# Performance work log

Hardware: AMD Instinct MI355X
Metric: run time of the kernel (lower is better)

Reference implementation:

```python
import jax, jax.numpy as jnp
import numpy as np

B, N, D = 8, 1024, 768
H, Y, M = 12, 64, 3072  # heads, head_dim, hopfield memories (4*D)
STEPS = 12
ALPHA = 0.1
EPS = 1e-5


def setup_inputs() -> dict:
    key = jax.random.key(0)
    k0, k1, k2, k3 = jax.random.split(key, 4)
    return {
        "x": jax.random.normal(k0, (B, N, D), dtype=jnp.float32),
        "gamma": jnp.ones((D,), dtype=jnp.float32),
        "beta_ln": jnp.zeros((D,), dtype=jnp.float32),
        "Wq": jax.random.normal(k1, (H, Y, D), dtype=jnp.float32) / np.float32(np.sqrt(D)),
        "Wk": jax.random.normal(k2, (H, Y, D), dtype=jnp.float32) / np.float32(np.sqrt(D)),
        "xi": jax.random.normal(k3, (M, D), dtype=jnp.float32) / np.float32(np.sqrt(D)),
    }


def _layernorm(x, gamma, beta_ln):
    mu = jnp.mean(x, axis=-1, keepdims=True)
    var = jnp.var(x, axis=-1, keepdims=True)
    return gamma * (x - mu) * jax.lax.rsqrt(var + EPS) + beta_ln


def _energy(g, Wq, Wk, xi):
    # Energy attention: E^ATT = -(1/beta) * sum_{h,q} logsumexp_k(beta * <K_hk, Q_hq>)
    q = jnp.einsum('hyd,bnd->bhny', Wq, g)
    k = jnp.einsum('hyd,bnd->bhny', Wk, g)
    beta = jnp.asarray(1.0 / np.sqrt(Y), g.dtype)
    scores = beta * jnp.einsum('bhky,bhqy->bhkq', k, q)  # [B,H,N_k,N_q]
    e_att = -(1.0 / beta) * jnp.sum(jax.nn.logsumexp(scores, axis=2))
    # Hopfield energy: E^HN = -0.5 * sum relu(g @ xi^T)^2
    h = jnp.einsum('bnd,md->bnm', g, xi)
    e_hn = -0.5 * jnp.sum(jnp.square(jax.nn.relu(h)))
    return e_att + e_hn


def reference(x, gamma, beta_ln, Wq, Wk, xi):
    grad_e = jax.grad(_energy)
    def step(xc, _):
        g = _layernorm(xc, gamma, beta_ln)
        # gradient taken at g (not chained through LayerNorm), then SGD update
        xc = xc - ALPHA * grad_e(g, Wq, Wk, xi)
        return xc, None
    out, _ = jax.lax.scan(step, x, None, length=STEPS)
    return out
```

## Files before the change

### kernel.cpp

```cpp
#include <hip/hip_runtime.h>
#include <math.h>

#define H_ 12
#define STEPS_ 12
#define ALPHA_ 0.1f
#define EPS_ 1e-5f
#define BETA_ 0.125f
#define NTOK 8192

typedef unsigned short u16;
typedef __attribute__((ext_vector_type(8))) u16 u16x8;
typedef __attribute__((ext_vector_type(4))) u16 u16x4;
typedef __attribute__((ext_vector_type(4))) float f32x4;
typedef __attribute__((ext_vector_type(8))) __bf16 bf16x8;

#define MFMA __builtin_amdgcn_mfma_f32_16x16x32_bf16

__device__ __forceinline__ u16 f2bf(float x) {
    unsigned u = __float_as_uint(x);
    u += 0x7FFFu + ((u >> 16) & 1u);
    return (u16)(u >> 16);
}
__device__ __forceinline__ float bf2f(u16 u) {
    return __uint_as_float(((unsigned)u) << 16);
}

__device__ __forceinline__ void gl2lds16(const u16* gsrc, u16* ldst) {
    __builtin_amdgcn_global_load_lds(
        (const __attribute__((address_space(1))) void*)gsrc,
        (__attribute__((address_space(3))) void*)ldst, 16, 0, 0);
}

#define RAW_BARRIER()   asm volatile("s_barrier" ::: "memory")
#define WAIT_VM(n)      asm volatile("s_waitcnt vmcnt(" #n ")" ::: "memory")

__global__ __launch_bounds__(256) void ln_kernel(const float* __restrict__ x,
    const float* __restrict__ gamma, const float* __restrict__ beta,
    u16* __restrict__ g)
{
    int row = blockIdx.x;
    const float* xr = x + (size_t)row * 768;
    u16* gr = g + (size_t)row * 768;
    int t = threadIdx.x;
    float v0 = xr[t], v1 = xr[t + 256], v2 = xr[t + 512];
    float s = v0 + v1 + v2;
    #pragma unroll
    for (int off = 32; off > 0; off >>= 1) s += __shfl_down(s, off);
    __shared__ float red[8];
    int wid = t >> 6, lane = t & 63;
    if (lane == 0) red[wid] = s;
    __syncthreads();
    if (t == 0) red[0] = (red[0] + red[1] + red[2] + red[3]) * (1.0f / 768.0f);
    __syncthreads();
    float mu = red[0];
    float d0 = v0 - mu, d1 = v1 - mu, d2 = v2 - mu;
    float ss = d0*d0 + d1*d1 + d2*d2;
    #pragma unroll
    for (int off = 32; off > 0; off >>= 1) ss += __shfl_down(ss, off);
    if (lane == 0) red[4 + wid] = ss;
    __syncthreads();
    if (t == 0) red[4] = rsqrtf((red[4] + red[5] + red[6] + red[7]) * (1.0f / 768.0f) + EPS_);
    __syncthreads();
    float rs = red[4];
    gr[t]       = f2bf(gamma[t]       * d0 * rs + beta[t]);
    gr[t + 256] = f2bf(gamma[t + 256] * d1 * rs + beta[t + 256]);
    gr[t + 512] = f2bf(gamma[t + 512] * d2 * rs + beta[t + 512]);
}

__global__ __launch_bounds__(192) void reduce_ln(const u16* __restrict__ part,
    float* __restrict__ xc, const float* __restrict__ gamma,
    const float* __restrict__ beta, u16* __restrict__ g)
{
    int row = blockIdx.x, t = threadIdx.x;
    const u16x4* p0 = (const u16x4*)(part + (size_t)row * 768);
    const u16x4* p1 = (const u16x4*)(part + (size_t)(8192 + row) * 768);
    f32x4* xr = (f32x4*)(xc + (size_t)row * 768);
    f32x4 v = xr[t];
    u16x4 a = p0[t], b = p1[t];
    #pragma unroll
    for (int e = 0; e < 4; ++e) v[e] = fmaf(ALPHA_, bf2f(a[e]) + bf2f(b[e]), v[e]);
    xr[t] = v;
    float s = (v[0] + v[1]) + (v[2] + v[3]);
    #pragma unroll
    for (int off = 32; off > 0; off >>= 1) s += __shfl_down(s, off);
    __shared__ float red[8];
    int wid = t >> 6, lane = t & 63;
    if (lane == 0) red[wid] = s;
    __syncthreads();
    if (t == 0) red[0] = (red[0] + red[1] + red[2]) * (1.0f / 768.0f);
    __syncthreads();
    float mu = red[0];
    f32x4 d;
    #pragma unroll
    for (int e = 0; e < 4; ++e) d[e] = v[e] - mu;
    float ss = (d[0]*d[0] + d[1]*d[1]) + (d[2]*d[2] + d[3]*d[3]);
    #pragma unroll
    for (int off = 32; off > 0; off >>= 1) ss += __shfl_down(ss, off);
    if (lane == 0) red[4 + wid] = ss;
    __syncthreads();
    if (t == 0) red[4] = rsqrtf((red[4] + red[5] + red[6]) * (1.0f / 768.0f) + EPS_);
    __syncthreads();
    float rs = red[4];
    const f32x4 gm = *(const f32x4*)&gamma[t * 4];
    const f32x4 bt = *(const f32x4*)&beta[t * 4];
    u16x4 o;
    #pragma unroll
    for (int e = 0; e < 4; ++e) o[e] = f2bf(fmaf(gm[e], d[e] * rs, bt[e]));
    *(u16x4*)&g[(size_t)row * 768 + t * 4] = o;
}

__global__ __launch_bounds__(256) void convert_bf(const float* __restrict__ src,
                                                  u16* __restrict__ dst, int n4)
{
    int i = blockIdx.x * 256 + threadIdx.x;
    if (i < n4) {
        f32x4 v = *(const f32x4*)&src[i * 4];
        u16x4 o;
        #pragma unroll
        for (int e = 0; e < 4; ++e) o[e] = f2bf(v[e]);
        *(u16x4*)&dst[i * 4] = o;
    }
}

__global__ __launch_bounds__(256) void transpose_bf(const float* __restrict__ Wq,
    const float* __restrict__ Wk, const float* __restrict__ xi, u16* __restrict__ out)
{
    __shared__ float tile[64][65];
    int rb = blockIdx.x * 64, cb = blockIdx.y * 64;
    const float* src;
    if (rb < 768) src = Wq + (size_t)rb * 768;
    else if (rb < 1536) src = Wk + (size_t)(rb - 768) * 768;
    else src = xi + (size_t)(rb - 1536) * 768;
    int t = threadIdx.x;
    #pragma unroll
    for (int it = 0; it < 4; ++it) {
        int r = (t >> 4) + 16 * it;
        f32x4 v = *(const f32x4*)&src[(size_t)r * 768 + cb + (t & 15) * 4];
        #pragma unroll
        for (int e = 0; e < 4; ++e) tile[r][(t & 15) * 4 + e] = v[e];
    }
    __syncthreads();
    #pragma unroll
    for (int it = 0; it < 4; ++it) {
        int cl = (t >> 4) + 16 * it;
        u16x4 o;
        #pragma unroll
        for (int e = 0; e < 4; ++e) o[e] = f2bf(tile[(t & 15) * 4 + e][cl]);
        *(u16x4*)&out[(size_t)(cb + cl) * 4608 + rb + (t & 15) * 4] = o;
    }
}

__global__ __launch_bounds__(512) void gemm_fwd(
    const u16* __restrict__ A,
    const u16* __restrict__ Bt,
    u16* __restrict__ qkb, u16* __restrict__ qkT, u16* __restrict__ midb)
{
    __shared__ __align__(16) u16 S[2][12288];
    const int t = threadIdx.x, w = t >> 6, l = t & 63, g = l >> 4, cid = l & 15;
    const int lr = l & 15, lc = l >> 4;
    const int flat = blockIdx.x;
    const int xcd = flat & 7, slot = flat >> 3;
    const int nid = slot / 4, mloc = slot % 4;
    const int bm = (xcd * 4 + mloc) * 256;
    const int bn = nid * 128;
    const int RO = (w >> 1) * 64, CO = (w & 1) * 64;
    f32x4 acc[4][4] = {};

    const u16* gp[3];
    int ld[3];
    #pragma unroll
    for (int j = 0; j < 3; ++j) {
        int c = 3 * w + j;
        if (c < 16) {
            gp[j] = A + (size_t)(bm + 16 * c + lr) * 768 + 8 * lc;
            ld[j] = (64 * c + l) * 8;
        } else {
            gp[j] = Bt + (size_t)(bn + 16 * (c - 16) + lr) * 768 + 8 * lc;
            ld[j] = 8192 + (64 * (c - 16) + l) * 8;
        }
    }

    auto stage = [&](int buf, int off) {
        #pragma unroll
        for (int j = 0; j < 3; ++j)
            gl2lds16(gp[j] + off, &S[buf][ld[j]]);
    };
    auto compute = [&](int buf) {
        bf16x8 af[4], bfr[4];
        #pragma unroll
        for (int i = 0; i < 4; ++i) af[i]  = *(const bf16x8*)&S[buf][(64 * ((RO >> 4) + i) + l) * 8];
        #pragma unroll
        for (int j = 0; j < 4; ++j) bfr[j] = *(const bf16x8*)&S[buf][8192 + (64 * ((CO >> 4) + j) + l) * 8];
        #pragma unroll
        for (int i = 0; i < 4; ++i)
            #pragma unroll
            for (int j = 0; j < 4; ++j)
                acc[i][j] = MFMA(af[i], bfr[j], acc[i][j], 0, 0, 0);
    };
    auto adv = [&]() { gp[0] += 64; gp[1] += 64; gp[2] += 64; };

    stage(0, 0); stage(1, 32);
    #pragma unroll 1
    for (int ii = 0; ii < 11; ++ii) {
        WAIT_VM(3); RAW_BARRIER(); compute(0); RAW_BARRIER(); stage(0, 64);
        WAIT_VM(3); RAW_BARRIER(); compute(1); RAW_BARRIER(); stage(1, 96);
        adv();
    }
    WAIT_VM(3); RAW_BARRIER(); compute(0);
    WAIT_VM(0); RAW_BARRIER(); compute(1);

    if (bn < 1536) {
        int bidx = bm >> 10;
        #pragma unroll
        for (int i = 0; i < 4; ++i) {
            int tok = bm + RO + 16 * i + 4 * g;
            #pragma unroll
            for (int j = 0; j < 4; ++j) {
                int col = bn + CO + 16 * j + cid;
                int sel = col >= 768 ? 1 : 0;
                int cc = col - 768 * sel;
                int hh = cc >> 6, yy = cc & 63;
                u16x4 tv;
                #pragma unroll
                for (int r = 0; r < 4; ++r) {
                    u16 bv = f2bf(acc[i][j][r]);
                    tv[r] = bv;
                    qkb[(size_t)(tok + r) * 1536 + col] = bv;
                }
                *(u16x4*)&qkT[((((size_t)bidx * 12 + hh) * 2 + sel) * 64 + yy) * 1024 + (tok & 1023)] = tv;
            }
        }
    } else {
        #pragma unroll
        for (int i = 0; i < 4; ++i)
            #pragma unroll
            for (int r = 0; r < 4; ++r) {
                size_t row = bm + RO + 16 * i + 4 * g + r;
                #pragma unroll
                for (int j = 0; j < 4; ++j) {
                    int col = bn + CO + 16 * j + cid;
                    midb[row * 4608 + col] = f2bf(fmaxf(acc[i][j][r], 0.0f));
                }
            }
    }
}

__global__ __launch_bounds__(256, 4) void gemm_upd(
    const u16* __restrict__ A,
    const u16* __restrict__ Bt,
    u16* __restrict__ part)
{
    __shared__ __align__(16) u16 As[2][4096];
    __shared__ __align__(16) u16 Bs[2][4096];
    const int t = threadIdx.x, w = t >> 6, l = t & 63, g = l >> 4, cid = l & 15;
    const int lr = l & 15, lc = l >> 4;
    const int flat = blockIdx.x;
    const int xcd = flat & 7, slot = flat >> 3;
    const int z = slot / 48, rem = slot % 48;
    const int mloc = rem / 6, n = rem % 6;
    const int bm = ((xcd << 3) + mloc) * 128, bn = n * 128;
    const int kbeg = z * 2304;
    const int RO = (w >> 1) * 64, CO = (w & 1) * 64;
    u16* out = part + (size_t)z * 8192 * 768;
    f32x4 acc[4][4] = {};

    const u16* ga0 = A  + (size_t)(bm + 32 * w + lr) * 4608 + kbeg + 8 * lc;
    const u16* ga1 = A  + (size_t)(bm + 32 * w + 16 + lr) * 4608 + kbeg + 8 * lc;
    const u16* gb0 = Bt + (size_t)(bn + 32 * w + lr) * 4608 + kbeg + 8 * lc;
    const u16* gb1 = Bt + (size_t)(bn + 32 * w + 16 + lr) * 4608 + kbeg + 8 * lc;

    auto stage = [&](int buf, int off) {
        gl2lds16(ga0 + off, &As[buf][(64 * (2 * w + 0) + l) * 8]);
        gl2lds16(ga1 + off, &As[buf][(64 * (2 * w + 1) + l) * 8]);
        gl2lds16(gb0 + off, &Bs[buf][(64 * (2 * w + 0) + l) * 8]);
        gl2lds16(gb1 + off, &Bs[buf][(64 * (2 * w + 1) + l) * 8]);
    };
    auto compute = [&](int buf) {
        bf16x8 af[4], bfr[4];
        #pragma unroll
        for (int i = 0; i < 4; ++i) af[i]  = *(const bf16x8*)&As[buf][(64 * ((RO >> 4) + i) + l) * 8];
        #pragma unroll
        for (int j = 0; j < 4; ++j) bfr[j] = *(const bf16x8*)&Bs[buf][(64 * ((CO >> 4) + j) + l) * 8];
        #pragma unroll
        for (int i = 0; i < 4; ++i)
            #pragma unroll
            for (int j = 0; j < 4; ++j)
                acc[i][j] = MFMA(af[i], bfr[j], acc[i][j], 0, 0, 0);
    };
    auto adv = [&]() { ga0 += 64; ga1 += 64; gb0 += 64; gb1 += 64; };

    stage(0, 0); stage(1, 32);
    #pragma unroll 1
    for (int ii = 0; ii < 35; ++ii) {
        WAIT_VM(4); RAW_BARRIER(); compute(0); RAW_BARRIER(); stage(0, 64);
        WAIT_VM(4); RAW_BARRIER(); compute(1); RAW_BARRIER(); stage(1, 96);
        adv();
    }
    WAIT_VM(4); RAW_BARRIER(); compute(0);
    WAIT_VM(0); RAW_BARRIER(); compute(1);

    #pragma unroll
    for (int i = 0; i < 4; ++i)
        #pragma unroll
        for (int r = 0; r < 4; ++r) {
            size_t row = bm + RO + 16 * i + 4 * g + r;
            #pragma unroll
            for (int j = 0; j < 4; ++j)
                out[row * 768 + bn + CO + 16 * j + cid] = f2bf(acc[i][j][r]);
        }
}

__global__ __launch_bounds__(256) void dq_kernel(const u16* __restrict__ qk,
    const u16* __restrict__ qkT, float* __restrict__ L, u16* __restrict__ mid)
{
    const int flat = blockIdx.x;
    const int xcd = flat & 7, slot = flat >> 3;
    const int bh = xcd * 12 + slot / 8;
    const int q0 = (slot % 8) << 7;
    const int b = bh / H_, h = bh % H_;
    const u16* qbase = qk + (size_t)b * 1024 * 1536 + h * 64;
    const u16* kbase = qbase + 768;
    const u16* ktg = qkT + ((size_t)bh * 2 + 1) * 64 * 1024;
    __shared__ __align__(16) u16 KB[2][8192];
    __shared__ __align__(16) u16 Ps[8192];
    const int t = threadIdx.x, w = t >> 6, l = t & 63, g = l >> 4, cid = l & 15;
    const int lr = l & 15, lc = l >> 4;

    #pragma unroll
    for (int h2 = 0; h2 < 2; ++h2)
        #pragma unroll
        for (int ch = 0; ch < 2; ++ch)
            gl2lds16(&qbase[(size_t)(q0 + 32 * w + 16 * h2 + lr) * 1536 + 32 * ch + 8 * lc],
                     &KB[0][(128 * (2 * w + h2) + 64 * ch + l) * 8]);
    __syncthreads();
    bf16x8 QF[2][2];
    #pragma unroll
    for (int jj = 0; jj < 2; ++jj)
        #pragma unroll
        for (int hh = 0; hh < 2; ++hh)
            QF[jj][hh] = *(const bf16x8*)&KB[0][(128 * (2 * w + jj) + 64 * hh + l) * 8];
    __syncthreads();

    auto stageK = [&](int buf, int kt) {
        #pragma unroll
        for (int ch = 0; ch < 2; ++ch) {
            gl2lds16(&kbase[(size_t)(kt * 64 + 16 * w + lr) * 1536 + 32 * ch + 8 * lc],
                     &KB[buf][(128 * w + 64 * ch + l) * 8]);
            gl2lds16(&ktg[(size_t)(16 * w + lr) * 1024 + kt * 64 + 32 * ch + 8 * lc],
                     &KB[buf][4096 + (128 * w + 64 * ch + l) * 8]);
        }
    };

    f32x4 acc[2][4] = {};
    float lrun[2] = {0.0f, 0.0f};

    stageK(0, 0); stageK(1, 1);
    #pragma unroll 1
    for (int kt = 0; kt < 16; ++kt) {
        if (kt == 15) { WAIT_VM(0); } else { WAIT_VM(4); }
        RAW_BARRIER();
        const int buf = kt & 1;
        const u16* Kn = &KB[buf][0];
        const u16* Kt = &KB[buf][4096];
        f32x4 s[4][2];
        #pragma unroll
        for (int i = 0; i < 4; ++i) {
            bf16x8 a0 = *(const bf16x8*)&Kn[(128 * i + l) * 8];
            bf16x8 a1 = *(const bf16x8*)&Kn[(128 * i + 64 + l) * 8];
            #pragma unroll
            for (int jj = 0; jj < 2; ++jj) {
                f32x4 z = {0.f, 0.f, 0.f, 0.f};
                z = MFMA(a0, QF[jj][0], z, 0, 0, 0);
                z = MFMA(a1, QF[jj][1], z, 0, 0, 0);
                s[i][jj] = z;
            }
        }
        #pragma unroll
        for (int jj = 0; jj < 2; ++jj) {
            float psum = 0.0f;
            #pragma unroll
            for (int i = 0; i < 4; ++i) {
                u16x4 pv;
                #pragma unroll
                for (int r = 0; r < 4; ++r) {
                    float p = __expf(s[i][jj][r] * BETA_);
                    psum += p;
                    pv[r] = f2bf(p);
                }
                *(u16x4*)&Ps[(128 * (2 * w + jj) + 32 * i + 16 * (g >> 1) + cid) * 8 + 4 * (g & 1)] = pv;
            }
            psum += __shfl_xor(psum, 16);
// ... 59 lines not shown
        for (int hh = 0; hh < 2; ++hh)
            KF[jj][hh] = *(const bf16x8*)&KB[0][(128 * (2 * w + jj) + 64 * hh + l) * 8];
    __syncthreads();

    auto stageQ = [&](int buf, int qt) {
        #pragma unroll
        for (int ch = 0; ch < 2; ++ch) {
            gl2lds16(&qbase[(size_t)(qt * 64 + 16 * w + lr) * 1536 + 32 * ch + 8 * lc],
                     &KB[buf][(128 * w + 64 * ch + l) * 8]);
            gl2lds16(&qtg[(size_t)(16 * w + lr) * 1024 + qt * 64 + 32 * ch + 8 * lc],
                     &KB[buf][4096 + (128 * w + 64 * ch + l) * 8]);
        }
    };

    f32x4 acc[2][4] = {};
    stageQ(0, 0); stageQ(1, 1);
    #pragma unroll 1
    for (int qt = 0; qt < 16; ++qt) {
        if (qt == 15) { WAIT_VM(0); } else { WAIT_VM(4); }
        RAW_BARRIER();
        const int buf = qt & 1;
        const u16* Qn = &KB[buf][0];
        const u16* Qt = &KB[buf][4096];
        #pragma unroll
        for (int i = 0; i < 4; ++i) {
            bf16x8 a0 = *(const bf16x8*)&Qn[(128 * i + l) * 8];
            bf16x8 a1 = *(const bf16x8*)&Qn[(128 * i + 64 + l) * 8];
            f32x4 lv = *(const f32x4*)&L[(size_t)bh * 1024 + qt * 64 + 16 * i + 4 * g];
            #pragma unroll
            for (int jj = 0; jj < 2; ++jj) {
                f32x4 z = {0.f, 0.f, 0.f, 0.f};
                z = MFMA(a0, KF[jj][0], z, 0, 0, 0);
                z = MFMA(a1, KF[jj][1], z, 0, 0, 0);
                u16x4 pv;
                #pragma unroll
                for (int r = 0; r < 4; ++r)
                    pv[r] = f2bf(__expf(fmaf(z[r], BETA_, -lv[r])));
                *(u16x4*)&Ps[(128 * (2 * w + jj) + 32 * i + 16 * (g >> 1) + cid) * 8 + 4 * (g & 1)] = pv;
            }
        }
        #pragma unroll
        for (int jj = 0; jj < 2; ++jj) {
            bf16x8 p0 = *(const bf16x8*)&Ps[(128 * (2 * w + jj) + l) * 8];
            bf16x8 p1 = *(const bf16x8*)&Ps[(128 * (2 * w + jj) + 64 + l) * 8];
            #pragma unroll
            for (int j = 0; j < 4; ++j) {
                acc[jj][j] = MFMA(p0, *(const bf16x8*)&Qt[(128 * j + l) * 8], acc[jj][j], 0, 0, 0);
                acc[jj][j] = MFMA(p1, *(const bf16x8*)&Qt[(128 * j + 64 + l) * 8], acc[jj][j], 0, 0, 0);
            }
        }
        RAW_BARRIER();
        if (qt + 2 < 16) stageQ(buf, qt + 2);
    }
    #pragma unroll
    for (int jj = 0; jj < 2; ++jj)
        #pragma unroll
        for (int r = 0; r < 4; ++r) {
            int row = k0 + 32 * w + 16 * jj + 4 * g + r;
            #pragma unroll
            for (int j = 0; j < 4; ++j)
                mid[(size_t)(b * 1024 + row) * 4608 + 768 + h * 64 + 16 * j + cid] = f2bf(acc[jj][j][r]);
        }
}

extern "C" void kernel_launch(void* const* d_in, const int* in_sizes, int n_in,
                              void* d_out, int out_size, void* d_ws, size_t ws_size,
                              hipStream_t stream)
{
    const float* x     = (const float*)d_in[0];
    const float* gamma = (const float*)d_in[1];
    const float* betap = (const float*)d_in[2];
    const float* Wq    = (const float*)d_in[3];
    const float* Wk    = (const float*)d_in[4];
    const float* xi    = (const float*)d_in[5];
    float* xc = (float*)d_out;

    char* p = (char*)d_ws;
    u16* wcat_bf  = (u16*)p; p += (size_t)4608 * 768 * 2;
    u16* wcatT_bf = (u16*)p; p += (size_t)768 * 4608 * 2;
    u16* g_bf     = (u16*)p; p += (size_t)NTOK * 768 * 2;
    u16* qk_bf    = (u16*)p; p += (size_t)NTOK * 1536 * 2;
    u16* qkT_bf   = (u16*)p; p += (size_t)96 * 2 * 64 * 1024 * 2;
    u16* mid_bf   = (u16*)p; p += (size_t)NTOK * 4608 * 2;
    u16* part     = (u16*)p; p += (size_t)2 * NTOK * 768 * 2;
    float* L      = (float*)p; p += (size_t)96 * 1024 * 4;
    (void)ws_size; (void)in_sizes; (void)n_in; (void)out_size;

    hipMemcpyAsync(xc, x, (size_t)NTOK * 768 * 4, hipMemcpyDeviceToDevice, stream);

    convert_bf<<<576, 256, 0, stream>>>(Wq, wcat_bf, 147456);
    convert_bf<<<576, 256, 0, stream>>>(Wk, wcat_bf + 768 * 768, 147456);
    convert_bf<<<2304, 256, 0, stream>>>(xi, wcat_bf + 2 * 768 * 768, 589824);
    transpose_bf<<<dim3(72, 12), 256, 0, stream>>>(Wq, Wk, xi, wcatT_bf);

    ln_kernel<<<NTOK, 256, 0, stream>>>(x, gamma, betap, g_bf);

    for (int step = 0; step < STEPS_; ++step) {
        gemm_fwd<<<1152, 512, 0, stream>>>(
            g_bf, wcat_bf, qk_bf, qkT_bf, mid_bf);
        dq_kernel<<<768, 256, 0, stream>>>(qk_bf, qkT_bf, L, mid_bf);
        dk_kernel<<<768, 256, 0, stream>>>(qk_bf, qkT_bf, L, mid_bf);
        gemm_upd<<<768, 256, 0, stream>>>(mid_bf, wcatT_bf, part);
        reduce_ln<<<NTOK, 192, 0, stream>>>(part, xc, gamma, betap, g_bf);
    }
}
```

Measured before the change: 3.709 ms.

## Triple-buffer GEMMs with 64-wide K tiles and retile update GEMM with 4-way split-K

Both projection GEMMs now stage 64-wide K slices into a three-slot LDS ring, keeping two loads in flight while computing on the third. The update GEMM becomes a 512-thread 256x128 tile with a 4-way K split, so reduce_ln now sums four bf16 partials. The partial buffer reuses the qk/qkT workspace, which is dead by then, so no extra memory is needed. The aim is to hide global-load latency and cut barriers per K step. In exchange, about 144KB of LDS per block allows only one block per CU, and split-K adds partial-buffer traffic.

```diff
diff --git a/kernel.cpp b/kernel.cpp
--- a/kernel.cpp
+++ b/kernel.cpp
@@ -74,11 +74,14 @@
     int row = blockIdx.x, t = threadIdx.x;
     const u16x4* p0 = (const u16x4*)(part + (size_t)row * 768);
     const u16x4* p1 = (const u16x4*)(part + (size_t)(8192 + row) * 768);
+    const u16x4* p2 = (const u16x4*)(part + (size_t)(16384 + row) * 768);
+    const u16x4* p3 = (const u16x4*)(part + (size_t)(24576 + row) * 768);
     f32x4* xr = (f32x4*)(xc + (size_t)row * 768);
     f32x4 v = xr[t];
-    u16x4 a = p0[t], b = p1[t];
-    #pragma unroll
-    for (int e = 0; e < 4; ++e) v[e] = fmaf(ALPHA_, bf2f(a[e]) + bf2f(b[e]), v[e]);
+    u16x4 a = p0[t], b = p1[t], c = p2[t], d4 = p3[t];
+    #pragma unroll
+    for (int e = 0; e < 4; ++e)
+        v[e] = fmaf(ALPHA_, (bf2f(a[e]) + bf2f(b[e])) + (bf2f(c[e]) + bf2f(d4[e])), v[e]);
     xr[t] = v;
     float s = (v[0] + v[1]) + (v[2] + v[3]);
     #pragma unroll
@@ -155,7 +158,7 @@
     const u16* __restrict__ Bt,
     u16* __restrict__ qkb, u16* __restrict__ qkT, u16* __restrict__ midb)
 {
-    __shared__ __align__(16) u16 S[2][12288];
+    __shared__ __align__(16) u16 S[3][24576];
     const int t = threadIdx.x, w = t >> 6, l = t & 63, g = l >> 4, cid = l & 15;
     const int lr = l & 15, lc = l >> 4;
     const int flat = blockIdx.x;
@@ -166,48 +169,56 @@
     const int RO = (w >> 1) * 64, CO = (w & 1) * 64;
     f32x4 acc[4][4] = {};
 
-    const u16* gp[3];
-    int ld[3];
-    #pragma unroll
-    for (int j = 0; j < 3; ++j) {
-        int c = 3 * w + j;
-        if (c < 16) {
-            gp[j] = A + (size_t)(bm + 16 * c + lr) * 768 + 8 * lc;
+    const u16* gp[6];
+    int ld[6];
+    #pragma unroll
+    for (int j = 0; j < 6; ++j) {
+        int c = 6 * w + j;
+        if (c < 32) {
+            gp[j] = A + (size_t)(bm + 16 * (c >> 1) + lr) * 768 + 32 * (c & 1) + 8 * lc;
             ld[j] = (64 * c + l) * 8;
         } else {
-            gp[j] = Bt + (size_t)(bn + 16 * (c - 16) + lr) * 768 + 8 * lc;
-            ld[j] = 8192 + (64 * (c - 16) + l) * 8;
-        }
-    }
-
-    auto stage = [&](int buf, int off) {
-        #pragma unroll
-        for (int j = 0; j < 3; ++j)
-            gl2lds16(gp[j] + off, &S[buf][ld[j]]);
+            int cb = c - 32;
+            gp[j] = Bt + (size_t)(bn + 16 * (cb >> 1) + lr) * 768 + 32 * (cb & 1) + 8 * lc;
+            ld[j] = 16384 + (64 * cb + l) * 8;
+        }
+    }
+
+    auto stage = [&](int buf, int koff) {
+        #pragma unroll
+        for (int j = 0; j < 6; ++j)
+            gl2lds16(gp[j] + koff, &S[buf][ld[j]]);
     };
     auto compute = [&](int buf) {
-        bf16x8 af[4], bfr[4];
-        #pragma unroll
-        for (int i = 0; i < 4; ++i) af[i]  = *(const bf16x8*)&S[buf][(64 * ((RO >> 4) + i) + l) * 8];
-        #pragma unroll
-        for (int j = 0; j < 4; ++j) bfr[j] = *(const bf16x8*)&S[buf][8192 + (64 * ((CO >> 4) + j) + l) * 8];
-        #pragma unroll
-        for (int i = 0; i < 4; ++i)
+        #pragma unroll
+        for (int h = 0; h < 2; ++h) {
+            bf16x8 af[4], bfr[4];
+            #pragma unroll
+            for (int i = 0; i < 4; ++i)
+                af[i]  = *(const bf16x8*)&S[buf][(64 * (2 * ((RO >> 4) + i) + h) + l) * 8];
             #pragma unroll
             for (int j = 0; j < 4; ++j)
-                acc[i][j] = MFMA(af[i], bfr[j], acc[i][j], 0, 0, 0);
+                bfr[j] = *(const bf16x8*)&S[buf][16384 + (64 * (2 * ((CO >> 4) + j) + h) + l) * 8];
+            #pragma unroll
+            for (int i = 0; i < 4; ++i)
+                #pragma unroll
+                for (int j = 0; j < 4; ++j)
+                    acc[i][j] = MFMA(af[i], bfr[j], acc[i][j], 0, 0, 0);
+        }
     };
-    auto adv = [&]() { gp[0] += 64; gp[1] += 64; gp[2] += 64; };
-
-    stage(0, 0); stage(1, 32);
+
+    stage(0, 0); stage(1, 64); stage(2, 128);
     #pragma unroll 1
-    for (int ii = 0; ii < 11; ++ii) {
-        WAIT_VM(3); RAW_BARRIER(); compute(0); RAW_BARRIER(); stage(0, 64);
-        WAIT_VM(3); RAW_BARRIER(); compute(1); RAW_BARRIER(); stage(1, 96);
-        adv();
-    }
-    WAIT_VM(3); RAW_BARRIER(); compute(0);
-    WAIT_VM(0); RAW_BARRIER(); compute(1);
+    for (int tt = 0; tt < 12; ++tt) {
+        if (tt < 10)      { WAIT_VM(12); }
+        else if (tt == 10){ WAIT_VM(6);  }
+        else              { WAIT_VM(0);  }
+        RAW_BARRIER();
+        const int buf = tt % 3;
+        compute(buf);
+        RAW_BARRIER();
+        if (tt < 9) stage(buf, 64 * (tt + 3));
+    }
 
     if (bn < 1536) {
         int bidx = bm >> 10;
@@ -245,59 +256,74 @@
     }
 }
 
-__global__ __launch_bounds__(256, 4) void gemm_upd(
+__global__ __launch_bounds__(512) void gemm_upd(
     const u16* __restrict__ A,
     const u16* __restrict__ Bt,
     u16* __restrict__ part)
 {
-    __shared__ __align__(16) u16 As[2][4096];
-    __shared__ __align__(16) u16 Bs[2][4096];
+    __shared__ __align__(16) u16 S[3][24576];
     const int t = threadIdx.x, w = t >> 6, l = t & 63, g = l >> 4, cid = l & 15;
     const int lr = l & 15, lc = l >> 4;
     const int flat = blockIdx.x;
     const int xcd = flat & 7, slot = flat >> 3;
-    const int z = slot / 48, rem = slot % 48;
-    const int mloc = rem / 6, n = rem % 6;
-    const int bm = ((xcd << 3) + mloc) * 128, bn = n * 128;
-    const int kbeg = z * 2304;
+    const int z = slot / 24, rem = slot % 24;
+    const int nid = rem / 4, mloc = rem % 4;
+    const int bm = (xcd * 4 + mloc) * 256, bn = nid * 128;
+    const int kbeg = z * 1152;
     const int RO = (w >> 1) * 64, CO = (w & 1) * 64;
     u16* out = part + (size_t)z * 8192 * 768;
     f32x4 acc[4][4] = {};
 
-    const u16* ga0 = A  + (size_t)(bm + 32 * w + lr) * 4608 + kbeg + 8 * lc;
-    const u16* ga1 = A  + (size_t)(bm + 32 * w + 16 + lr) * 4608 + kbeg + 8 * lc;
-    const u16* gb0 = Bt + (size_t)(bn + 32 * w + lr) * 4608 + kbeg + 8 * lc;
-    const u16* gb1 = Bt + (size_t)(bn + 32 * w + 16 + lr) * 4608 + kbeg + 8 * lc;
-
-    auto stage = [&](int buf, int off) {
-        gl2lds16(ga0 + off, &As[buf][(64 * (2 * w + 0) + l) * 8]);
-        gl2lds16(ga1 + off, &As[buf][(64 * (2 * w + 1) + l) * 8]);
-        gl2lds16(gb0 + off, &Bs[buf][(64 * (2 * w + 0) + l) * 8]);
-        gl2lds16(gb1 + off, &Bs[buf][(64 * (2 * w + 1) + l) * 8]);
+    const u16* gp[6];
+    int ld[6];
+    #pragma unroll
+    for (int j = 0; j < 6; ++j) {
+        int c = 6 * w + j;
+        if (c < 32) {
+            gp[j] = A + (size_t)(bm + 16 * (c >> 1) + lr) * 4608 + kbeg + 32 * (c & 1) + 8 * lc;
+            ld[j] = (64 * c + l) * 8;
+        } else {
+            int cb = c - 32;
+            gp[j] = Bt + (size_t)(bn + 16 * (cb >> 1) + lr) * 4608 + kbeg + 32 * (cb & 1) + 8 * lc;
+            ld[j] = 16384 + (64 * cb + l) * 8;
+        }
+    }
+
+    auto stage = [&](int buf, int koff) {
+        #pragma unroll
+        for (int j = 0; j < 6; ++j)
+            gl2lds16(gp[j] + koff, &S[buf][ld[j]]);
     };
     auto compute = [&](int buf) {
-        bf16x8 af[4], bfr[4];
-        #pragma unroll
-        for (int i = 0; i < 4; ++i) af[i]  = *(const bf16x8*)&As[buf][(64 * ((RO >> 4) + i) + l) * 8];
-        #pragma unroll
-        for (int j = 0; j < 4; ++j) bfr[j] = *(const bf16x8*)&Bs[buf][(64 * ((CO >> 4) + j) + l) * 8];
-        #pragma unroll
-        for (int i = 0; i < 4; ++i)
+        #pragma unroll
+        for (int h = 0; h < 2; ++h) {
+            bf16x8 af[4], bfr[4];
+            #pragma unroll
+            for (int i = 0; i < 4; ++i)
+                af[i]  = *(const bf16x8*)&S[buf][(64 * (2 * ((RO >> 4) + i) + h) + l) * 8];
             #pragma unroll
             for (int j = 0; j < 4; ++j)
-                acc[i][j] = MFMA(af[i], bfr[j], acc[i][j], 0, 0, 0);
+                bfr[j] = *(const bf16x8*)&S[buf][16384 + (64 * (2 * ((CO >> 4) + j) + h) + l) * 8];
+            #pragma unroll
+            for (int i = 0; i < 4; ++i)
+                #pragma unroll
+                for (int j = 0; j < 4; ++j)
+                    acc[i][j] = MFMA(af[i], bfr[j], acc[i][j], 0, 0, 0);
+        }
     };
-    auto adv = [&]() { ga0 += 64; ga1 += 64; gb0 += 64; gb1 += 64; };
-
-    stage(0, 0); stage(1, 32);
+
+    stage(0, 0); stage(1, 64); stage(2, 128);
     #pragma unroll 1
-    for (int ii = 0; ii < 35; ++ii) {
-        WAIT_VM(4); RAW_BARRIER(); compute(0); RAW_BARRIER(); stage(0, 64);
-        WAIT_VM(4); RAW_BARRIER(); compute(1); RAW_BARRIER(); stage(1, 96);
-        adv();
-    }
-    WAIT_VM(4); RAW_BARRIER(); compute(0);
-    WAIT_VM(0); RAW_BARRIER(); compute(1);
+    for (int tt = 0; tt < 18; ++tt) {
+        if (tt < 16)      { WAIT_VM(12); }
+        else if (tt == 16){ WAIT_VM(6);  }
+        else              { WAIT_VM(0);  }
+        RAW_BARRIER();
+        const int buf = tt % 3;
+        compute(buf);
+        RAW_BARRIER();
+        if (tt < 15) stage(buf, 64 * (tt + 3));
+    }
 
     #pragma unroll
     for (int i = 0; i < 4; ++i)
@@ -532,8 +558,8 @@
     u16* qk_bf    = (u16*)p; p += (size_t)NTOK * 1536 * 2;
     u16* qkT_bf   = (u16*)p; p += (size_t)96 * 2 * 64 * 1024 * 2;
     u16* mid_bf   = (u16*)p; p += (size_t)NTOK * 4608 * 2;
-    u16* part     = (u16*)p; p += (size_t)2 * NTOK * 768 * 2;
     float* L      = (float*)p; p += (size_t)96 * 1024 * 4;
+    u16* part = qk_bf;
     (void)ws_size; (void)in_sizes; (void)n_in; (void)out_size;
 
     hipMemcpyAsync(xc, x, (size_t)NTOK * 768 * 4, hipMemcpyDeviceToDevice, stream);
@@ -550,7 +576,7 @@
             g_bf, wcat_bf, qk_bf, qkT_bf, mid_bf);
         dq_kernel<<<768, 256, 0, stream>>>(qk_bf, qkT_bf, L, mid_bf);
         dk_kernel<<<768, 256, 0, stream>>>(qk_bf, qkT_bf, L, mid_bf);
-        gemm_upd<<<768, 256, 0, stream>>>(mid_bf, wcatT_bf, part);
+        gemm_upd<<<768, 512, 0, stream>>>(mid_bf, wcatT_bf, part);
         reduce_ln<<<NTOK, 192, 0, stream>>>(part, xc, gamma, betap, g_bf);
     }
 }
```

Result: no change. 3.662 ms (-1.3%).

## Use 256x256 tiles with interleaved staging in both GEMMs, four-way split-K

Applied to the files above, without the earlier changes.

Both the forward GEMM and the update GEMM move to 256x256 output tiles per 512-thread block, with 64-wide K stages. Each K stage is split into four MFMA quadrants, with global-to-LDS loads interleaved between them, raised wave priority during MFMA, and scheduling fences. The update GEMM goes from a two-way to a four-way split-K, so reduce_ln now sums four partials, and the partial buffer reuses the qk workspace. The aim is more operand reuse per byte loaded into LDS and better overlap of loads with compute. The cost is higher register and LDS pressure (64 KB per buffer pair) and fewer blocks in flight.

```diff
diff --git a/kernel.cpp b/kernel.cpp
--- a/kernel.cpp
+++ b/kernel.cpp
@@ -33,6 +33,16 @@
 
 #define RAW_BARRIER()   asm volatile("s_barrier" ::: "memory")
 #define WAIT_VM(n)      asm volatile("s_waitcnt vmcnt(" #n ")" ::: "memory")
+#define SCHED_FENCE()   __builtin_amdgcn_sched_barrier(0)
+
+#define QUAD(IB, JB, BR) \
+    { _Pragma("unroll") \
+      for (int i_ = 0; i_ < 4; ++i_) { \
+        _Pragma("unroll") \
+        for (int j_ = 0; j_ < 2; ++j_) { \
+            acc[(IB)+i_][(JB)+j_] = MFMA(afr[i_][0], BR[j_][0], acc[(IB)+i_][(JB)+j_], 0,0,0); \
+            acc[(IB)+i_][(JB)+j_] = MFMA(afr[i_][1], BR[j_][1], acc[(IB)+i_][(JB)+j_], 0,0,0); \
+        } } }
 
 __global__ __launch_bounds__(256) void ln_kernel(const float* __restrict__ x,
     const float* __restrict__ gamma, const float* __restrict__ beta,
@@ -74,11 +84,14 @@
     int row = blockIdx.x, t = threadIdx.x;
     const u16x4* p0 = (const u16x4*)(part + (size_t)row * 768);
     const u16x4* p1 = (const u16x4*)(part + (size_t)(8192 + row) * 768);
+    const u16x4* p2 = (const u16x4*)(part + (size_t)(16384 + row) * 768);
+    const u16x4* p3 = (const u16x4*)(part + (size_t)(24576 + row) * 768);
     f32x4* xr = (f32x4*)(xc + (size_t)row * 768);
     f32x4 v = xr[t];
-    u16x4 a = p0[t], b = p1[t];
-    #pragma unroll
-    for (int e = 0; e < 4; ++e) v[e] = fmaf(ALPHA_, bf2f(a[e]) + bf2f(b[e]), v[e]);
+    u16x4 a = p0[t], b = p1[t], c = p2[t], d4 = p3[t];
+    #pragma unroll
+    for (int e = 0; e < 4; ++e)
+        v[e] = fmaf(ALPHA_, (bf2f(a[e]) + bf2f(b[e])) + (bf2f(c[e]) + bf2f(d4[e])), v[e]);
     xr[t] = v;
     float s = (v[0] + v[1]) + (v[2] + v[3]);
     #pragma unroll
@@ -155,68 +168,96 @@
     const u16* __restrict__ Bt,
     u16* __restrict__ qkb, u16* __restrict__ qkT, u16* __restrict__ midb)
 {
-    __shared__ __align__(16) u16 S[2][12288];
+    __shared__ __align__(16) u16 S[2][32768];
     const int t = threadIdx.x, w = t >> 6, l = t & 63, g = l >> 4, cid = l & 15;
     const int lr = l & 15, lc = l >> 4;
+    const int wm = w >> 2, wn = w & 3;
     const int flat = blockIdx.x;
     const int xcd = flat & 7, slot = flat >> 3;
-    const int nid = slot / 4, mloc = slot % 4;
+    const int nid = slot >> 2, mloc = slot & 3;
     const int bm = (xcd * 4 + mloc) * 256;
-    const int bn = nid * 128;
-    const int RO = (w >> 1) * 64, CO = (w & 1) * 64;
-    f32x4 acc[4][4] = {};
-
-    const u16* gp[3];
-    int ld[3];
-    #pragma unroll
-    for (int j = 0; j < 3; ++j) {
-        int c = 3 * w + j;
-        if (c < 16) {
-            gp[j] = A + (size_t)(bm + 16 * c + lr) * 768 + 8 * lc;
-            ld[j] = (64 * c + l) * 8;
-        } else {
-            gp[j] = Bt + (size_t)(bn + 16 * (c - 16) + lr) * 768 + 8 * lc;
-            ld[j] = 8192 + (64 * (c - 16) + l) * 8;
-        }
-    }
-
-    auto stage = [&](int buf, int off) {
-        #pragma unroll
-        for (int j = 0; j < 3; ++j)
-            gl2lds16(gp[j] + off, &S[buf][ld[j]]);
+    const int bn = nid * 256;
+    const int NT = 12;
+
+    const u16* aA[2]; const u16* bB[2];
+    int ldA[2], ldB[2];
+    #pragma unroll
+    for (int hh = 0; hh < 2; ++hh) {
+        aA[hh] = A  + (size_t)(bm + 16 * (hh * 8 + w) + lr) * 768 + 8 * lc;
+        bB[hh] = Bt + (size_t)(bn + 16 * (hh * 8 + w) + lr) * 768 + 8 * lc;
+        ldA[hh] = (128 * (hh * 8 + w) + l) * 8;
+        ldB[hh] = 16384 + (128 * (hh * 8 + w) + l) * 8;
+    }
+    auto stageA = [&](int buf, int hh, int k0) {
+        gl2lds16(aA[hh] + k0,      &S[buf][ldA[hh]]);
+        gl2lds16(aA[hh] + k0 + 32, &S[buf][ldA[hh] + 512]);
     };
-    auto compute = [&](int buf) {
-        bf16x8 af[4], bfr[4];
-        #pragma unroll
-        for (int i = 0; i < 4; ++i) af[i]  = *(const bf16x8*)&S[buf][(64 * ((RO >> 4) + i) + l) * 8];
-        #pragma unroll
-        for (int j = 0; j < 4; ++j) bfr[j] = *(const bf16x8*)&S[buf][8192 + (64 * ((CO >> 4) + j) + l) * 8];
-        #pragma unroll
-        for (int i = 0; i < 4; ++i)
-            #pragma unroll
-            for (int j = 0; j < 4; ++j)
-                acc[i][j] = MFMA(af[i], bfr[j], acc[i][j], 0, 0, 0);
+    auto stageB = [&](int buf, int hh, int k0) {
+        gl2lds16(bB[hh] + k0,      &S[buf][ldB[hh]]);
+        gl2lds16(bB[hh] + k0 + 32, &S[buf][ldB[hh] + 512]);
     };
-    auto adv = [&]() { gp[0] += 64; gp[1] += 64; gp[2] += 64; };
-
-    stage(0, 0); stage(1, 32);
+
+    f32x4 acc[8][4] = {};
+    bf16x8 afr[4][2], b0[2][2], b1[2][2];
+
+    stageB(0, 0, 0); stageB(0, 1, 0); stageA(0, 0, 0); stageA(0, 1, 0);
+    stageB(1, 0, 64); stageB(1, 1, 64);
+    WAIT_VM(4); RAW_BARRIER();
+
     #pragma unroll 1
-    for (int ii = 0; ii < 11; ++ii) {
-        WAIT_VM(3); RAW_BARRIER(); compute(0); RAW_BARRIER(); stage(0, 64);
-        WAIT_VM(3); RAW_BARRIER(); compute(1); RAW_BARRIER(); stage(1, 96);
-        adv();
-    }
-    WAIT_VM(3); RAW_BARRIER(); compute(0);
-    WAIT_VM(0); RAW_BARRIER(); compute(1);
+    for (int tt = 0; tt < NT; ++tt) {
+        const int bf = tt & 1, ob = bf ^ 1;
+        const u16* Sa = &S[bf][0];
+        const u16* Sb = &S[bf][16384];
+        #define LDS_A(ii, hh) (*(const bf16x8*)&Sa[(wm*1024 + (ii)*128 + (hh)*64 + l) * 8])
+        #define LDS_B(jj, hh) (*(const bf16x8*)&Sb[((wn*4 + (jj))*128 + (hh)*64 + l) * 8])
+        #pragma unroll
+        for (int i = 0; i < 4; ++i) { afr[i][0] = LDS_A(i, 0); afr[i][1] = LDS_A(i, 1); }
+        #pragma unroll
+        for (int j = 0; j < 2; ++j) { b0[j][0] = LDS_B(j, 0); b0[j][1] = LDS_B(j, 1); }
+        if (tt + 1 < NT) stageA(ob, 0, 64 * (tt + 1));
+        RAW_BARRIER();
+        __builtin_amdgcn_s_setprio(1);
+        QUAD(0, 0, b0);
+        __builtin_amdgcn_s_setprio(0);
+        SCHED_FENCE(); RAW_BARRIER();
+        #pragma unroll
+        for (int j = 0; j < 2; ++j) { b1[j][0] = LDS_B(2 + j, 0); b1[j][1] = LDS_B(2 + j, 1); }
+        if (tt + 1 < NT) stageA(ob, 1, 64 * (tt + 1));
+        RAW_BARRIER();
+        __builtin_amdgcn_s_setprio(1);
+        QUAD(0, 2, b1);
+        __builtin_amdgcn_s_setprio(0);
+        SCHED_FENCE(); RAW_BARRIER();
+        #pragma unroll
+        for (int i = 0; i < 4; ++i) { afr[i][0] = LDS_A(4 + i, 0); afr[i][1] = LDS_A(4 + i, 1); }
+        if (tt + 2 < NT) stageB(bf, 0, 64 * (tt + 2));
+        RAW_BARRIER();
+        __builtin_amdgcn_s_setprio(1);
+        QUAD(4, 2, b1);
+        __builtin_amdgcn_s_setprio(0);
+        SCHED_FENCE(); RAW_BARRIER();
+        if (tt + 2 < NT) stageB(bf, 1, 64 * (tt + 2));
+        RAW_BARRIER();
+        __builtin_amdgcn_s_setprio(1);
+        QUAD(4, 0, b0);
+        __builtin_amdgcn_s_setprio(0);
+        SCHED_FENCE();
+        if (tt < NT - 2)       { WAIT_VM(4); }
+        else if (tt == NT - 2) { WAIT_VM(0); }
+        RAW_BARRIER();
+        #undef LDS_A
+        #undef LDS_B
+    }
 
     if (bn < 1536) {
         int bidx = bm >> 10;
         #pragma unroll
-        for (int i = 0; i < 4; ++i) {
-            int tok = bm + RO + 16 * i + 4 * g;
+        for (int i = 0; i < 8; ++i) {
+            int tok = bm + wm * 128 + 16 * i + 4 * g;
             #pragma unroll
             for (int j = 0; j < 4; ++j) {
-                int col = bn + CO + 16 * j + cid;
+                int col = bn + wn * 64 + 16 * j + cid;
                 int sel = col >= 768 ? 1 : 0;
                 int cc = col - 768 * sel;
                 int hh = cc >> 6, yy = cc & 63;
@@ -232,81 +273,116 @@
         }
     } else {
         #pragma unroll
-        for (int i = 0; i < 4; ++i)
+        for (int i = 0; i < 8; ++i)
             #pragma unroll
             for (int r = 0; r < 4; ++r) {
-                size_t row = bm + RO + 16 * i + 4 * g + r;
+                size_t row = bm + wm * 128 + 16 * i + 4 * g + r;
                 #pragma unroll
                 for (int j = 0; j < 4; ++j) {
-                    int col = bn + CO + 16 * j + cid;
+                    int col = bn + wn * 64 + 16 * j + cid;
                     midb[row * 4608 + col] = f2bf(fmaxf(acc[i][j][r], 0.0f));
                 }
             }
     }
 }
 
-__global__ __launch_bounds__(256, 4) void gemm_upd(
+__global__ __launch_bounds__(512) void gemm_upd(
     const u16* __restrict__ A,
     const u16* __restrict__ Bt,
     u16* __restrict__ part)
 {
-    __shared__ __align__(16) u16 As[2][4096];
-    __shared__ __align__(16) u16 Bs[2][4096];
+    __shared__ __align__(16) u16 S[2][32768];
     const int t = threadIdx.x, w = t >> 6, l = t & 63, g = l >> 4, cid = l & 15;
     const int lr = l & 15, lc = l >> 4;
+    const int wm = w >> 2, wn = w & 3;
     const int flat = blockIdx.x;
     const int xcd = flat & 7, slot = flat >> 3;
-    const int z = slot / 48, rem = slot % 48;
-    const int mloc = rem / 6, n = rem % 6;
-    const int bm = ((xcd << 3) + mloc) * 128, bn = n * 128;
-    const int kbeg = z * 2304;
-    const int RO = (w >> 1) * 64, CO = (w & 1) * 64;
+    const int z = slot / 12, rem = slot % 12;
+    const int nid = rem >> 2, mloc = rem & 3;
+    const int bm = (xcd * 4 + mloc) * 256, bn = nid * 256;
+    const int kbeg = z * 1152;
+    const int NT = 18;
     u16* out = part + (size_t)z * 8192 * 768;
-    f32x4 acc[4][4] = {};
-
-    const u16* ga0 = A  + (size_t)(bm + 32 * w + lr) * 4608 + kbeg + 8 * lc;
-    const u16* ga1 = A  + (size_t)(bm + 32 * w + 16 + lr) * 4608 + kbeg + 8 * lc;
-    const u16* gb0 = Bt + (size_t)(bn + 32 * w + lr) * 4608 + kbeg + 8 * lc;
-    const u16* gb1 = Bt + (size_t)(bn + 32 * w + 16 + lr) * 4608 + kbeg + 8 * lc;
-
-    auto stage = [&](int buf, int off) {
-        gl2lds16(ga0 + off, &As[buf][(64 * (2 * w + 0) + l) * 8]);
-        gl2lds16(ga1 + off, &As[buf][(64 * (2 * w + 1) + l) * 8]);
-        gl2lds16(gb0 + off, &Bs[buf][(64 * (2 * w + 0) + l) * 8]);
-        gl2lds16(gb1 + off, &Bs[buf][(64 * (2 * w + 1) + l) * 8]);
+
+    const u16* aA[2]; const u16* bB[2];
+    int ldA[2], ldB[2];
+    #pragma unroll
+    for (int hh = 0; hh < 2; ++hh) {
+        aA[hh] = A  + (size_t)(bm + 16 * (hh * 8 + w) + lr) * 4608 + kbeg + 8 * lc;
+        bB[hh] = Bt + (size_t)(bn + 16 * (hh * 8 + w) + lr) * 4608 + kbeg + 8 * lc;
+        ldA[hh] = (128 * (hh * 8 + w) + l) * 8;
+        ldB[hh] = 16384 + (128 * (hh * 8 + w) + l) * 8;
+    }
+    auto stageA = [&](int buf, int hh, int k0) {
+        gl2lds16(aA[hh] + k0,      &S[buf][ldA[hh]]);
+        gl2lds16(aA[hh] + k0 + 32, &S[buf][ldA[hh] + 512]);
     };
-    auto compute = [&](int buf) {
-        bf16x8 af[4], bfr[4];
-        #pragma unroll
-        for (int i = 0; i < 4; ++i) af[i]  = *(const bf16x8*)&As[buf][(64 * ((RO >> 4) + i) + l) * 8];
-        #pragma unroll
-        for (int j = 0; j < 4; ++j) bfr[j] = *(const bf16x8*)&Bs[buf][(64 * ((CO >> 4) + j) + l) * 8];
-        #pragma unroll
-        for (int i = 0; i < 4; ++i)
+    auto stageB = [&](int buf, int hh, int k0) {
+        gl2lds16(bB[hh] + k0,      &S[buf][ldB[hh]]);
+        gl2lds16(bB[hh] + k0 + 32, &S[buf][ldB[hh] + 512]);
+    };
+
+    f32x4 acc[8][4] = {};
+    bf16x8 afr[4][2], b0[2][2], b1[2][2];
+
+    stageB(0, 0, 0); stageB(0, 1, 0); stageA(0, 0, 0); stageA(0, 1, 0);
+    stageB(1, 0, 64); stageB(1, 1, 64);
+    WAIT_VM(4); RAW_BARRIER();
+
+    #pragma unroll 1
+    for (int tt = 0; tt < NT; ++tt) {
+        const int bf = tt & 1, ob = bf ^ 1;
+        const u16* Sa = &S[bf][0];
+        const u16* Sb = &S[bf][16384];
+        #define LDS_A(ii, hh) (*(const bf16x8*)&Sa[(wm*1024 + (ii)*128 + (hh)*64 + l) * 8])
+        #define LDS_B(jj, hh) (*(const bf16x8*)&Sb[((wn*4 + (jj))*128 + (hh)*64 + l) * 8])
+        #pragma unroll
+        for (int i = 0; i < 4; ++i) { afr[i][0] = LDS_A(i, 0); afr[i][1] = LDS_A(i, 1); }
+        #pragma unroll
+        for (int j = 0; j < 2; ++j) { b0[j][0] = LDS_B(j, 0); b0[j][1] = LDS_B(j, 1); }
+        if (tt + 1 < NT) stageA(ob, 0, 64 * (tt + 1));
+        RAW_BARRIER();
+        __builtin_amdgcn_s_setprio(1);
+        QUAD(0, 0, b0);
+        __builtin_amdgcn_s_setprio(0);
+        SCHED_FENCE(); RAW_BARRIER();
+        #pragma unroll
+        for (int j = 0; j < 2; ++j) { b1[j][0] = LDS_B(2 + j, 0); b1[j][1] = LDS_B(2 + j, 1); }
+        if (tt + 1 < NT) stageA(ob, 1, 64 * (tt + 1));
+        RAW_BARRIER();
+        __builtin_amdgcn_s_setprio(1);
+        QUAD(0, 2, b1);
+        __builtin_amdgcn_s_setprio(0);
+        SCHED_FENCE(); RAW_BARRIER();
+        #pragma unroll
+        for (int i = 0; i < 4; ++i) { afr[i][0] = LDS_A(4 + i, 0); afr[i][1] = LDS_A(4 + i, 1); }
+        if (tt + 2 < NT) stageB(bf, 0, 64 * (tt + 2));
+        RAW_BARRIER();
+        __builtin_amdgcn_s_setprio(1);
+        QUAD(4, 2, b1);
+        __builtin_amdgcn_s_setprio(0);
+        SCHED_FENCE(); RAW_BARRIER();
+        if (tt + 2 < NT) stageB(bf, 1, 64 * (tt + 2));
+        RAW_BARRIER();
+        __builtin_amdgcn_s_setprio(1);
+        QUAD(4, 0, b0);
+        __builtin_amdgcn_s_setprio(0);
+        SCHED_FENCE();
+        if (tt < NT - 2)       { WAIT_VM(4); }
+        else if (tt == NT - 2) { WAIT_VM(0); }
+        RAW_BARRIER();
+        #undef LDS_A
+        #undef LDS_B
+    }
+
+    #pragma unroll
+    for (int i = 0; i < 8; ++i)
+        #pragma unroll
+        for (int r = 0; r < 4; ++r) {
+            size_t row = bm + wm * 128 + 16 * i + 4 * g + r;
             #pragma unroll
             for (int j = 0; j < 4; ++j)
-                acc[i][j] = MFMA(af[i], bfr[j], acc[i][j], 0, 0, 0);
-    };
-    auto adv = [&]() { ga0 += 64; ga1 += 64; gb0 += 64; gb1 += 64; };
-
-    stage(0, 0); stage(1, 32);
-    #pragma unroll 1
-    for (int ii = 0; ii < 35; ++ii) {
-        WAIT_VM(4); RAW_BARRIER(); compute(0); RAW_BARRIER(); stage(0, 64);
-        WAIT_VM(4); RAW_BARRIER(); compute(1); RAW_BARRIER(); stage(1, 96);
-        adv();
-    }
-    WAIT_VM(4); RAW_BARRIER(); compute(0);
-    WAIT_VM(0); RAW_BARRIER(); compute(1);
-
-    #pragma unroll
-    for (int i = 0; i < 4; ++i)
-        #pragma unroll
-        for (int r = 0; r < 4; ++r) {
-            size_t row = bm + RO + 16 * i + 4 * g + r;
-            #pragma unroll
-            for (int j = 0; j < 4; ++j)
-                out[row * 768 + bn + CO + 16 * j + cid] = f2bf(acc[i][j][r]);
+                out[row * 768 + bn + wn * 64 + 16 * j + cid] = f2bf(acc[i][j][r]);
         }
 }
 
@@ -532,8 +608,8 @@
     u16* qk_bf    = (u16*)p; p += (size_t)NTOK * 1536 * 2;
     u16* qkT_bf   = (u16*)p; p += (size_t)96 * 2 * 64 * 1024 * 2;
     u16* mid_bf   = (u16*)p; p += (size_t)NTOK * 4608 * 2;
-    u16* part     = (u16*)p; p += (size_t)2 * NTOK * 768 * 2;
     float* L      = (float*)p; p += (size_t)96 * 1024 * 4;
+    u16* part = qk_bf;
     (void)ws_size; (void)in_sizes; (void)n_in; (void)out_size;
 
     hipMemcpyAsync(xc, x, (size_t)NTOK * 768 * 4, hipMemcpyDeviceToDevice, stream);
@@ -546,11 +622,11 @@
     ln_kernel<<<NTOK, 256, 0, stream>>>(x, gamma, betap, g_bf);
 
     for (int step = 0; step < STEPS_; ++step) {
-        gemm_fwd<<<1152, 512, 0, stream>>>(
+        gemm_fwd<<<576, 512, 0, stream>>>(
             g_bf, wcat_bf, qk_bf, qkT_bf, mid_bf);
         dq_kernel<<<768, 256, 0, stream>>>(qk_bf, qkT_bf, L, mid_bf);
         dk_kernel<<<768, 256, 0, stream>>>(qk_bf, qkT_bf, L, mid_bf);
-        gemm_upd<<<768, 256, 0, stream>>>(mid_bf, wcatT_bf, part);
+        gemm_upd<<<384, 512, 0, stream>>>(mid_bf, wcatT_bf, part);
         reduce_ln<<<NTOK, 192, 0, stream>>>(part, xc, gamma, betap, g_bf);
     }
 }
```

Result: faster. 3.359 ms (-9.4%).

## Shrink forward GEMM tile, simplify double-buffered pipelines, alias partial buffer onto qk

Applied to the files above, without the earlier changes.

The forward GEMM goes from 512-thread blocks on 256x128 tiles to 256-thread blocks on 128x128 tiles, doubling the grid. Both GEMMs now use a single-prefetch double-buffer loop with one wait and barrier per K-step instead of the two-stage WAIT_VM pipeline. The split-K partial buffer is aliased onto the qk buffer, which is dead by then, to cut workspace. The simpler pipeline gives less latency hiding per step, and the 4-blocks-per-CU launch bound on gemm_upd is dropped.

```diff
diff --git a/kernel.cpp b/kernel.cpp
--- a/kernel.cpp
+++ b/kernel.cpp
@@ -150,64 +150,58 @@
     }
 }
 
-__global__ __launch_bounds__(512) void gemm_fwd(
+
+__global__ __launch_bounds__(256) void gemm_fwd(
     const u16* __restrict__ A,
     const u16* __restrict__ Bt,
     u16* __restrict__ qkb, u16* __restrict__ qkT, u16* __restrict__ midb)
 {
-    __shared__ __align__(16) u16 S[2][12288];
+    __shared__ __align__(16) u16 S[2][8192];
     const int t = threadIdx.x, w = t >> 6, l = t & 63, g = l >> 4, cid = l & 15;
     const int lr = l & 15, lc = l >> 4;
     const int flat = blockIdx.x;
     const int xcd = flat & 7, slot = flat >> 3;
-    const int nid = slot / 4, mloc = slot % 4;
-    const int bm = (xcd * 4 + mloc) * 256;
+    const int nid = slot >> 3, mloc = slot & 7;
+    const int bm = (xcd * 8 + mloc) * 128;
     const int bn = nid * 128;
+    const int NT = 24;
     const int RO = (w >> 1) * 64, CO = (w & 1) * 64;
+
+    const u16* gp[4]; int ld[4];
+    #pragma unroll
+    for (int j = 0; j < 4; ++j) {
+        int c = 4 * w + j;
+        if (c < 8) { gp[j] = A  + (size_t)(bm + 16 * c + lr) * 768 + 8 * lc;
+                     ld[j] = c * 512; }
+        else       { gp[j] = Bt + (size_t)(bn + 16 * (c - 8) + lr) * 768 + 8 * lc;
+                     ld[j] = 4096 + (c - 8) * 512; }
+    }
+
     f32x4 acc[4][4] = {};
 
-    const u16* gp[3];
-    int ld[3];
-    #pragma unroll
-    for (int j = 0; j < 3; ++j) {
-        int c = 3 * w + j;
-        if (c < 16) {
-            gp[j] = A + (size_t)(bm + 16 * c + lr) * 768 + 8 * lc;
-            ld[j] = (64 * c + l) * 8;
-        } else {
-            gp[j] = Bt + (size_t)(bn + 16 * (c - 16) + lr) * 768 + 8 * lc;
-            ld[j] = 8192 + (64 * (c - 16) + l) * 8;
-        }
-    }
-
-    auto stage = [&](int buf, int off) {
-        #pragma unroll
-        for (int j = 0; j < 3; ++j)
-            gl2lds16(gp[j] + off, &S[buf][ld[j]]);
-    };
-    auto compute = [&](int buf) {
-        bf16x8 af[4], bfr[4];
-        #pragma unroll
-        for (int i = 0; i < 4; ++i) af[i]  = *(const bf16x8*)&S[buf][(64 * ((RO >> 4) + i) + l) * 8];
-        #pragma unroll
-        for (int j = 0; j < 4; ++j) bfr[j] = *(const bf16x8*)&S[buf][8192 + (64 * ((CO >> 4) + j) + l) * 8];
+    #pragma unroll
+    for (int j = 0; j < 4; ++j) gl2lds16(gp[j], &S[0][ld[j]]);
+    WAIT_VM(0); RAW_BARRIER();
+
+    #pragma unroll 1
+    for (int tt = 0; tt < NT; ++tt) {
+        const int bf = tt & 1, ob = bf ^ 1;
+        if (tt + 1 < NT) {
+            #pragma unroll
+            for (int j = 0; j < 4; ++j) gl2lds16(gp[j] + 32 * (tt + 1), &S[ob][ld[j]]);
+        }
+        bf16x8 af[4], bq[4];
+        #pragma unroll
+        for (int i = 0; i < 4; ++i) af[i] = *(const bf16x8*)&S[bf][(((RO >> 4) + i) * 512) + l * 8];
+        #pragma unroll
+        for (int j = 0; j < 4; ++j) bq[j] = *(const bf16x8*)&S[bf][4096 + (((CO >> 4) + j) * 512) + l * 8];
         #pragma unroll
         for (int i = 0; i < 4; ++i)
             #pragma unroll
             for (int j = 0; j < 4; ++j)
-                acc[i][j] = MFMA(af[i], bfr[j], acc[i][j], 0, 0, 0);
-    };
-    auto adv = [&]() { gp[0] += 64; gp[1] += 64; gp[2] += 64; };
-
-    stage(0, 0); stage(1, 32);
-    #pragma unroll 1
-    for (int ii = 0; ii < 11; ++ii) {
-        WAIT_VM(3); RAW_BARRIER(); compute(0); RAW_BARRIER(); stage(0, 64);
-        WAIT_VM(3); RAW_BARRIER(); compute(1); RAW_BARRIER(); stage(1, 96);
-        adv();
-    }
-    WAIT_VM(3); RAW_BARRIER(); compute(0);
-    WAIT_VM(0); RAW_BARRIER(); compute(1);
+                acc[i][j] = MFMA(af[i], bq[j], acc[i][j], 0, 0, 0);
+        WAIT_VM(0); RAW_BARRIER();
+    }
 
     if (bn < 1536) {
         int bidx = bm >> 10;
@@ -245,59 +239,59 @@
     }
 }
 
-__global__ __launch_bounds__(256, 4) void gemm_upd(
+__global__ __launch_bounds__(256) void gemm_upd(
     const u16* __restrict__ A,
     const u16* __restrict__ Bt,
     u16* __restrict__ part)
 {
-    __shared__ __align__(16) u16 As[2][4096];
-    __shared__ __align__(16) u16 Bs[2][4096];
+    __shared__ __align__(16) u16 S[2][8192];
     const int t = threadIdx.x, w = t >> 6, l = t & 63, g = l >> 4, cid = l & 15;
     const int lr = l & 15, lc = l >> 4;
     const int flat = blockIdx.x;
     const int xcd = flat & 7, slot = flat >> 3;
     const int z = slot / 48, rem = slot % 48;
-    const int mloc = rem / 6, n = rem % 6;
-    const int bm = ((xcd << 3) + mloc) * 128, bn = n * 128;
+    const int nid = rem >> 3, mloc = rem & 7;
+    const int bm = (xcd * 8 + mloc) * 128, bn = nid * 128;
     const int kbeg = z * 2304;
+    const int NT = 72;
     const int RO = (w >> 1) * 64, CO = (w & 1) * 64;
     u16* out = part + (size_t)z * 8192 * 768;
+
+    const u16* gp[4]; int ld[4];
+    #pragma unroll
+    for (int j = 0; j < 4; ++j) {
+        int c = 4 * w + j;
+        if (c < 8) { gp[j] = A  + (size_t)(bm + 16 * c + lr) * 4608 + kbeg + 8 * lc;
+                     ld[j] = c * 512; }
+        else       { gp[j] = Bt + (size_t)(bn + 16 * (c - 8) + lr) * 4608 + kbeg + 8 * lc;
+                     ld[j] = 4096 + (c - 8) * 512; }
+    }
+
     f32x4 acc[4][4] = {};
 
-    const u16* ga0 = A  + (size_t)(bm + 32 * w + lr) * 4608 + kbeg + 8 * lc;
-    const u16* ga1 = A  + (size_t)(bm + 32 * w + 16 + lr) * 4608 + kbeg + 8 * lc;
-    const u16* gb0 = Bt + (size_t)(bn + 32 * w + lr) * 4608 + kbeg + 8 * lc;
-    const u16* gb1 = Bt + (size_t)(bn + 32 * w + 16 + lr) * 4608 + kbeg + 8 * lc;
-
-    auto stage = [&](int buf, int off) {
-        gl2lds16(ga0 + off, &As[buf][(64 * (2 * w + 0) + l) * 8]);
-        gl2lds16(ga1 + off, &As[buf][(64 * (2 * w + 1) + l) * 8]);
-        gl2lds16(gb0 + off, &Bs[buf][(64 * (2 * w + 0) + l) * 8]);
-        gl2lds16(gb1 + off, &Bs[buf][(64 * (2 * w + 1) + l) * 8]);
-    };
-    auto compute = [&](int buf) {
-        bf16x8 af[4], bfr[4];
-        #pragma unroll
-        for (int i = 0; i < 4; ++i) af[i]  = *(const bf16x8*)&As[buf][(64 * ((RO >> 4) + i) + l) * 8];
-        #pragma unroll
-        for (int j = 0; j < 4; ++j) bfr[j] = *(const bf16x8*)&Bs[buf][(64 * ((CO >> 4) + j) + l) * 8];
+    #pragma unroll
+    for (int j = 0; j < 4; ++j) gl2lds16(gp[j], &S[0][ld[j]]);
+    WAIT_VM(0); RAW_BARRIER();
+
+    #pragma unroll 1
+    for (int tt = 0; tt < NT; ++tt) {
+        const int bf = tt & 1, ob = bf ^ 1;
+        if (tt + 1 < NT) {
+            #pragma unroll
+            for (int j = 0; j < 4; ++j) gl2lds16(gp[j] + 32 * (tt + 1), &S[ob][ld[j]]);
+        }
+        bf16x8 af[4], bq[4];
+        #pragma unroll
+        for (int i = 0; i < 4; ++i) af[i] = *(const bf16x8*)&S[bf][(((RO >> 4) + i) * 512) + l * 8];
+        #pragma unroll
+        for (int j = 0; j < 4; ++j) bq[j] = *(const bf16x8*)&S[bf][4096 + (((CO >> 4) + j) * 512) + l * 8];
         #pragma unroll
         for (int i = 0; i < 4; ++i)
             #pragma unroll
             for (int j = 0; j < 4; ++j)
-                acc[i][j] = MFMA(af[i], bfr[j], acc[i][j], 0, 0, 0);
-    };
-    auto adv = [&]() { ga0 += 64; ga1 += 64; gb0 += 64; gb1 += 64; };
-
-    stage(0, 0); stage(1, 32);
-    #pragma unroll 1
-    for (int ii = 0; ii < 35; ++ii) {
-        WAIT_VM(4); RAW_BARRIER(); compute(0); RAW_BARRIER(); stage(0, 64);
-        WAIT_VM(4); RAW_BARRIER(); compute(1); RAW_BARRIER(); stage(1, 96);
-        adv();
-    }
-    WAIT_VM(4); RAW_BARRIER(); compute(0);
-    WAIT_VM(0); RAW_BARRIER(); compute(1);
+                acc[i][j] = MFMA(af[i], bq[j], acc[i][j], 0, 0, 0);
+        WAIT_VM(0); RAW_BARRIER();
+    }
 
     #pragma unroll
     for (int i = 0; i < 4; ++i)
@@ -532,8 +526,8 @@
     u16* qk_bf    = (u16*)p; p += (size_t)NTOK * 1536 * 2;
     u16* qkT_bf   = (u16*)p; p += (size_t)96 * 2 * 64 * 1024 * 2;
     u16* mid_bf   = (u16*)p; p += (size_t)NTOK * 4608 * 2;
-    u16* part     = (u16*)p; p += (size_t)2 * NTOK * 768 * 2;
     float* L      = (float*)p; p += (size_t)96 * 1024 * 4;
+    u16* part = qk_bf;
     (void)ws_size; (void)in_sizes; (void)n_in; (void)out_size;
 
     hipMemcpyAsync(xc, x, (size_t)NTOK * 768 * 4, hipMemcpyDeviceToDevice, stream);
@@ -546,7 +540,7 @@
     ln_kernel<<<NTOK, 256, 0, stream>>>(x, gamma, betap, g_bf);
 
     for (int step = 0; step < STEPS_; ++step) {
-        gemm_fwd<<<1152, 512, 0, stream>>>(
+        gemm_fwd<<<2304, 256, 0, stream>>>(
             g_bf, wcat_bf, qk_bf, qkT_bf, mid_bf);
         dq_kernel<<<768, 256, 0, stream>>>(qk_bf, qkT_bf, L, mid_bf);
         dk_kernel<<<768, 256, 0, stream>>>(qk_bf, qkT_bf, L, mid_bf);
```

After: 4.039 ms. +8.9%, slower.
